# Optimization experiments

Hardware: AMD Instinct MI355X
Metric: run time of the kernel (lower is better)

## Reference

```python
import jax, jax.numpy as jnp
import numpy as np

E = 1024      # embed_dim
H = 16        # num_heads
DH = E // H   # head_dim = 64
B, T = 2, 2048


def setup_inputs() -> dict:
    key = jax.random.key(0)
    ks = jax.random.split(key, 9)
    s = 0.02
    return {
        "hidden_states": jax.random.normal(ks[0], (B, T, E), dtype=jnp.float32),
        "Wq": jax.random.normal(ks[1], (E, E), dtype=jnp.float32) * s,
        "bq": jax.random.normal(ks[2], (E,), dtype=jnp.float32) * s,
        "Wk": jax.random.normal(ks[3], (E, E), dtype=jnp.float32) * s,
        "bk": jax.random.normal(ks[4], (E,), dtype=jnp.float32) * s,
        "Wv": jax.random.normal(ks[5], (E, E), dtype=jnp.float32) * s,
        "bv": jax.random.normal(ks[6], (E,), dtype=jnp.float32) * s,
        "Wo": jax.random.normal(ks[7], (E, E), dtype=jnp.float32) * s,
        "bo": jax.random.normal(ks[8], (E,), dtype=jnp.float32) * s,
    }


def reference(hidden_states, Wq, bq, Wk, bk, Wv, bv, Wo, bo):
    # Faithful to the source, including its bugs:
    #  - q scaled by head_dim**-0.5 AND scores divided by sqrt(head_dim) -> net 1/head_dim
    #  - softmax output assigned to a dead variable; raw scores used for AV matmul
    b, t, _ = hidden_states.shape
    scaling = DH ** -0.5
    q = (hidden_states @ Wq.T + bq) * scaling            # [b, t, E]
    k = hidden_states @ Wk.T + bk
    v = hidden_states @ Wv.T + bv

    def split_heads(x):  # [b, t, E] -> [b, H, t, DH]
        return x.reshape(b, t, H, DH).transpose(0, 2, 1, 3)

    qh, kh, vh = split_heads(q), split_heads(k), split_heads(v)
    attn = jnp.einsum("bhtd,bhsd->bhts", qh, kh) / jnp.sqrt(jnp.float32(DH))
    # (softmax computed in source but its result is discarded)
    out = jnp.einsum("bhts,bhsd->bhtd", attn, vh)        # [b, H, t, DH]
    out = out.transpose(0, 2, 1, 3).reshape(b, t, E)
    return out @ Wo.T + bo
```

## Files before the change

kernel.cpp:

```cpp
#include <hip/hip_runtime.h>

#define E_  1024
#define H_  16
#define B_  2
#define T_  2048
#define BT_ (B_*T_)

typedef __bf16 bf16x8 __attribute__((ext_vector_type(8)));
typedef float  f32x4  __attribute__((ext_vector_type(4)));
typedef unsigned short u16x8 __attribute__((ext_vector_type(8)));

static __device__ __forceinline__ unsigned short f2bf(float x){
  unsigned int u = __float_as_uint(x);
  u += 0x7fffu + ((u >> 16) & 1u);
  return (unsigned short)(u >> 16);
}
static __device__ __forceinline__ float bf2f(unsigned short s){
  return __uint_as_float(((unsigned int)s) << 16);
}

static __device__ __forceinline__ void gld16(const unsigned short* g, unsigned short* l){
  __builtin_amdgcn_global_load_lds(
      (const __attribute__((address_space(1))) void*)g,
      (__attribute__((address_space(3))) void*)l, 16, 0, 0);
}

__global__ __launch_bounds__(256)
void cast_all(const float* __restrict__ hidden,
              const float* __restrict__ Wq, const float* __restrict__ Wk,
              const float* __restrict__ Wv, const float* __restrict__ Wo,
              unsigned short* __restrict__ hb,
              unsigned short* __restrict__ wqkv, unsigned short* __restrict__ wob){
  int bid = blockIdx.x;
  const float* src;
  unsigned short* dst;
  int off;
  if (bid < 2048) {
    src = hidden; dst = hb; off = bid * 2048 + threadIdx.x * 8;
  } else {
    int w = (bid - 2048) >> 9;
    off = ((bid - 2048) & 511) * 2048 + threadIdx.x * 8;
    src = (w==0) ? Wq : (w==1) ? Wk : (w==2) ? Wv : Wo;
    dst = (w==3) ? wob : (wqkv + (size_t)w * 1048576);
  }
  float4 v0 = *(const float4*)(src + off);
  float4 v1 = *(const float4*)(src + off + 4);
  u16x8 o;
  o[0]=f2bf(v0.x); o[1]=f2bf(v0.y); o[2]=f2bf(v0.z); o[3]=f2bf(v0.w);
  o[4]=f2bf(v1.x); o[5]=f2bf(v1.y); o[6]=f2bf(v1.z); o[7]=f2bf(v1.w);
  *(u16x8*)(dst + off) = o;
}

__global__ __launch_bounds__(256)
void gemm_qkv(const unsigned short* __restrict__ A,
              const unsigned short* __restrict__ Wqkv,
              const float* __restrict__ bq, const float* __restrict__ bk,
              const float* __restrict__ bv,
              unsigned short* __restrict__ Q, unsigned short* __restrict__ Ko,
              unsigned short* __restrict__ Vo)
{
  __shared__ unsigned short As[4096];
  __shared__ unsigned short Bs[4096];
  const int tid = threadIdx.x;
  const int wv = tid >> 6, ln = tid & 63;
  const int wr = wv >> 1, wc = wv & 1;
  const int lr = ln & 15;
  const int lk8 = (ln >> 4) * 8;
  const int bm = blockIdx.x, bn = blockIdx.y;
  const size_t arow0 = (size_t)bm * 128;
  const size_t brow0 = (size_t)bn * 128;
  const int K = 1024;

  f32x4 acc[4][4];
  #pragma unroll
  for (int m = 0; m < 4; ++m)
    #pragma unroll
    for (int n = 0; n < 4; ++n) acc[m][n] = (f32x4){0.f,0.f,0.f,0.f};

  for (int k0 = 0; k0 < K; k0 += 32) {
    #pragma unroll
    for (int i = 0; i < 2; ++i) {
      int c = i*256 + wv*64 + ln;
      int row = c >> 2, off = (c & 3) * 8;
      gld16(A    + (arow0 + row) * K + k0 + off, As + (size_t)(i*256 + wv*64) * 8);
      gld16(Wqkv + (brow0 + row) * K + k0 + off, Bs + (size_t)(i*256 + wv*64) * 8);
    }
    __syncthreads();
    bf16x8 af[4], bf[4];
    #pragma unroll
    for (int m = 0; m < 4; ++m) af[m] = *(const bf16x8*)&As[(wr*64 + m*16 + lr)*32 + lk8];
    #pragma unroll
    for (int n = 0; n < 4; ++n) bf[n] = *(const bf16x8*)&Bs[(wc*64 + n*16 + lr)*32 + lk8];
    #pragma unroll
    for (int m = 0; m < 4; ++m)
      #pragma unroll
      for (int n = 0; n < 4; ++n)
        acc[m][n] = __builtin_amdgcn_mfma_f32_16x16x32_bf16(af[m], bf[n], acc[m][n], 0, 0, 0);
    __syncthreads();
  }

  const int which = bn >> 3;
  const float* bias = (which==0) ? bq : (which==1) ? bk : bv;
  unsigned short* Out = (which==0) ? Q : (which==1) ? Ko : Vo;
  const float scale = (which==0) ? 0.125f : 1.0f;
  #pragma unroll
  for (int n = 0; n < 4; ++n) {
    int col = (bn & 7)*128 + wc*64 + n*16 + lr;
    float bvv = bias[col];
    #pragma unroll
    for (int m = 0; m < 4; ++m) {
      int row0 = bm*128 + wr*64 + m*16 + (ln >> 4) * 4;
      #pragma unroll
      for (int r = 0; r < 4; ++r)
        Out[(size_t)(row0 + r) * 1024 + col] = f2bf((acc[m][n][r] + bvv) * scale);
    }
  }
}

__global__ __launch_bounds__(256)
void gemm_o(const unsigned short* __restrict__ A,
            const unsigned short* __restrict__ Bw,
            const float* __restrict__ bias, float* __restrict__ C)
{
  __shared__ unsigned short As[4096];
  __shared__ unsigned short Bs[2048];
  const int tid = threadIdx.x;
  const int wv = tid >> 6, ln = tid & 63;
  const int wr = wv >> 1, wc = wv & 1;
  const int lr = ln & 15;
  const int lk8 = (ln >> 4) * 8;
  const int bm = blockIdx.x, bn = blockIdx.y;
  const size_t arow0 = (size_t)bm * 128;
  const size_t brow0 = (size_t)bn * 64;
  const int K = 1024;

  f32x4 acc[4][2];
  #pragma unroll
  for (int m = 0; m < 4; ++m)
    #pragma unroll
    for (int n = 0; n < 2; ++n) acc[m][n] = (f32x4){0.f,0.f,0.f,0.f};

  for (int k0 = 0; k0 < K; k0 += 32) {
    #pragma unroll
    for (int i = 0; i < 2; ++i) {
      int c = i*256 + wv*64 + ln;
      int row = c >> 2, off = (c & 3) * 8;
      gld16(A + (arow0 + row) * K + k0 + off, As + (size_t)(i*256 + wv*64) * 8);
    }
    { int c = wv*64 + ln; int row = c >> 2, off = (c & 3) * 8;
      gld16(Bw + (brow0 + row) * K + k0 + off, Bs + (size_t)(wv*64) * 8); }
    __syncthreads();
    bf16x8 af[4], bf[2];
    #pragma unroll
    for (int m = 0; m < 4; ++m) af[m] = *(const bf16x8*)&As[(wr*64 + m*16 + lr)*32 + lk8];
    #pragma unroll
    for (int n = 0; n < 2; ++n) bf[n] = *(const bf16x8*)&Bs[(wc*32 + n*16 + lr)*32 + lk8];
    #pragma unroll
    for (int m = 0; m < 4; ++m)
      #pragma unroll
      for (int n = 0; n < 2; ++n)
        acc[m][n] = __builtin_amdgcn_mfma_f32_16x16x32_bf16(af[m], bf[n], acc[m][n], 0, 0, 0);
    __syncthreads();
  }

  #pragma unroll
  for (int n = 0; n < 2; ++n) {
    int col = bn*64 + wc*32 + n*16 + lr;
    float bvv = bias[col];
    #pragma unroll
    for (int m = 0; m < 4; ++m) {
      int row0 = bm*128 + wr*64 + m*16 + (ln >> 4) * 4;
      #pragma unroll
      for (int r = 0; r < 4; ++r)
        C[(size_t)(row0 + r) * 1024 + col] = acc[m][n][r] + bvv;
    }
  }
}

__global__ __launch_bounds__(256)
void ktv_partial(const unsigned short* __restrict__ Kmat,
                 const unsigned short* __restrict__ Vmat,
                 float* __restrict__ Mpart)
{
  __shared__ float Ks[32][64];
  __shared__ float Vs[32][64];
  const int tid   = threadIdx.x;
  const int bh    = blockIdx.x;
  const int chunk = blockIdx.y;
  const int b = bh >> 4, h = bh & 15;
  const int d2  = tid & 63;
  const int d1b = (tid >> 6) * 16;
  float acc[16];
  #pragma unroll
  for (int i = 0; i < 16; ++i) acc[i] = 0.f;
  const int row = tid >> 3, off = (tid & 7) * 8;
  const size_t base = ((size_t)b * T_) * E_ + (size_t)h * 64;

  for (int t0 = chunk * 128; t0 < chunk * 128 + 128; t0 += 32) {
    u16x8 kv = *(const u16x8*)(Kmat + base + (size_t)(t0 + row) * E_ + off);
    u16x8 vv = *(const u16x8*)(Vmat + base + (size_t)(t0 + row) * E_ + off);
    #pragma unroll
    for (int j = 0; j < 8; ++j) { Ks[row][off+j] = bf2f(kv[j]); Vs[row][off+j] = bf2f(vv[j]); }
    __syncthreads();
    for (int tt = 0; tt < 32; ++tt) {
      float vvv = Vs[tt][d2];
      #pragma unroll
      for (int i = 0; i < 16; ++i) acc[i] += Ks[tt][d1b + i] * vvv;
    }
    __syncthreads();
  }
  float* mp = Mpart + ((size_t)bh * 16 + chunk) * 4096;
  #pragma unroll
  for (int i = 0; i < 16; ++i) mp[(d1b + i) * 64 + d2] = acc[i];
}

__global__ __launch_bounds__(256)
void ktv_reduce(const float* __restrict__ Mpart, float* __restrict__ Mfin){
  const int bh = blockIdx.x;
  for (int i = threadIdx.x; i < 4096; i += 256) {
    float s = 0.f;
    #pragma unroll
    for (int c = 0; c < 16; ++c) s += Mpart[((size_t)bh * 16 + c) * 4096 + i];
    Mfin[(size_t)bh * 4096 + i] = s * 0.125f;
  }
}

__global__ __launch_bounds__(256)
void qm_kernel(const unsigned short* __restrict__ Q,
               const float* __restrict__ Mfin,
               unsigned short* __restrict__ O)
{
  __shared__ float Ms[64][64];
  __shared__ float Qs[32][64];
  const int tid = threadIdx.x;
  const int rb  = blockIdx.x;
  const int h   = blockIdx.y;
  const int b   = rb >> 6;
  const int t0  = (rb & 63) * 32;
  const float* mf = Mfin + ((size_t)(b * 16 + h)) * 4096;
  for (int i = tid; i < 4096; i += 256) Ms[i >> 6][i & 63] = mf[i];
  const int row = tid >> 3, off = (tid & 7) * 8;
  const size_t base = ((size_t)b * T_) * E_ + (size_t)h * 64;
  u16x8 qv = *(const u16x8*)(Q + base + (size_t)(t0 + row) * E_ + off);
  #pragma unroll
  for (int j = 0; j < 8; ++j) Qs[row][off + j] = bf2f(qv[j]);
  __syncthreads();
  const int d2 = tid & 63;
  const int r0 = (tid >> 6) * 8;
  for (int rr = r0; rr < r0 + 8; ++rr) {
    float s = 0.f;
    #pragma unroll
    for (int d1 = 0; d1 < 64; ++d1) s += Qs[rr][d1] * Ms[d1][d2];
    O[base + (size_t)(t0 + rr) * E_ + d2] = f2bf(s);
  }
}

extern "C" void kernel_launch(void* const* d_in, const int* in_sizes, int n_in,
                              void* d_out, int out_size, void* d_ws, size_t ws_size,
                              hipStream_t stream)
{
  const float* hidden = (const float*)d_in[0];
  const float* Wq = (const float*)d_in[1];
  const float* bq = (const float*)d_in[2];
  const float* Wk = (const float*)d_in[3];
  const float* bk = (const float*)d_in[4];
  const float* Wv = (const float*)d_in[5];
  const float* bv = (const float*)d_in[6];
  const float* Wo = (const float*)d_in[7];
  const float* bo = (const float*)d_in[8];
  float* out = (float*)d_out;

  const size_t SZ_ACT = (size_t)BT_ * E_;
  const size_t SZ_W   = (size_t)E_ * E_;

  char* p = (char*)d_ws;
  unsigned short* hb   = (unsigned short*)p; p += SZ_ACT * 2;
  unsigned short* wqkv = (unsigned short*)p; p += SZ_W * 3 * 2;
  unsigned short* wob  = (unsigned short*)p; p += SZ_W * 2;
  unsigned short* qb   = (unsigned short*)p; p += SZ_ACT * 2;
  unsigned short* kb   = (unsigned short*)p; p += SZ_ACT * 2;
  unsigned short* vb   = (unsigned short*)p; p += SZ_ACT * 2;
  unsigned short* ob   = (unsigned short*)p; p += SZ_ACT * 2;
  float* Mpart = (float*)p; p += (size_t)32 * 16 * 4096 * 4;
  float* Mfin  = (float*)p; p += (size_t)32 * 4096 * 4;

  cast_all<<<4096, 256, 0, stream>>>(hidden, Wq, Wk, Wv, Wo, hb, wqkv, wob);

  gemm_qkv<<<dim3(32, 24), 256, 0, stream>>>(hb, wqkv, bq, bk, bv, qb, kb, vb);

  ktv_partial<<<dim3(32, 16), 256, 0, stream>>>(kb, vb, Mpart);
  ktv_reduce <<<32, 256, 0, stream>>>(Mpart, Mfin);
  qm_kernel  <<<dim3(128, 16), 256, 0, stream>>>(qb, Mfin, ob);

  gemm_o<<<dim3(32, 16), 256, 0, stream>>>(ob, wob, bo, out);
}
```

Before: 106.0 us.

## Use bf16 MFMA for Q·M product with transposed bf16 M matrix

The reduce kernel now writes the final per-head 64x64 K^T V matrix transposed and rounded to bf16, staged through a padded LDS tile. The Q·M kernel drops its LDS staging and scalar FMA loop. Each wave instead loads Q and M^T fragments directly from global memory and issues 16x16x32 bf16 MFMA instructions. This removes LDS traffic and scalar compute in that stage, at the cost of an extra bf16 rounding of M that may add numerical error.

```diff
diff --git a/kernel.cpp b/kernel.cpp
--- a/kernel.cpp
+++ b/kernel.cpp
@@ -215,43 +215,66 @@
 }
 
 __global__ __launch_bounds__(256)
-void ktv_reduce(const float* __restrict__ Mpart, float* __restrict__ Mfin){
+void ktv_reduce(const float* __restrict__ Mpart, unsigned short* __restrict__ MfinT){
+  __shared__ float Tl[64][65];
   const int bh = blockIdx.x;
-  for (int i = threadIdx.x; i < 4096; i += 256) {
+  const int tid = threadIdx.x;
+  #pragma unroll
+  for (int j = 0; j < 16; ++j) {
+    int i = j*256 + tid;
     float s = 0.f;
     #pragma unroll
     for (int c = 0; c < 16; ++c) s += Mpart[((size_t)bh * 16 + c) * 4096 + i];
-    Mfin[(size_t)bh * 4096 + i] = s * 0.125f;
+    Tl[i & 63][i >> 6] = s * 0.125f;
+  }
+  __syncthreads();
+  unsigned short* o = MfinT + (size_t)bh * 4096;
+  #pragma unroll
+  for (int j = 0; j < 16; ++j) {
+    int i = j*256 + tid;
+    o[i] = f2bf(Tl[i >> 6][i & 63]);
   }
 }
 
 __global__ __launch_bounds__(256)
 void qm_kernel(const unsigned short* __restrict__ Q,
-               const float* __restrict__ Mfin,
+               const unsigned short* __restrict__ MfinT,
                unsigned short* __restrict__ O)
 {
-  __shared__ float Ms[64][64];
-  __shared__ float Qs[32][64];
   const int tid = threadIdx.x;
-  const int rb  = blockIdx.x;
-  const int h   = blockIdx.y;
-  const int b   = rb >> 6;
-  const int t0  = (rb & 63) * 32;
-  const float* mf = Mfin + ((size_t)(b * 16 + h)) * 4096;
-  for (int i = tid; i < 4096; i += 256) Ms[i >> 6][i & 63] = mf[i];
-  const int row = tid >> 3, off = (tid & 7) * 8;
+  const int wv = tid >> 6, ln = tid & 63;
+  const int lr = ln & 15, lk8 = (ln >> 4) * 8;
+  const int rb = blockIdx.x;
+  const int h  = blockIdx.y;
+  const int b  = rb >> 6;
+  const int t0 = (rb & 63) * 32;
   const size_t base = ((size_t)b * T_) * E_ + (size_t)h * 64;
-  u16x8 qv = *(const u16x8*)(Q + base + (size_t)(t0 + row) * E_ + off);
-  #pragma unroll
-  for (int j = 0; j < 8; ++j) Qs[row][off + j] = bf2f(qv[j]);
-  __syncthreads();
-  const int d2 = tid & 63;
-  const int r0 = (tid >> 6) * 8;
-  for (int rr = r0; rr < r0 + 8; ++rr) {
-    float s = 0.f;
-    #pragma unroll
-    for (int d1 = 0; d1 < 64; ++d1) s += Qs[rr][d1] * Ms[d1][d2];
-    O[base + (size_t)(t0 + rr) * E_ + d2] = f2bf(s);
+  const unsigned short* mt = MfinT + ((size_t)(b * 16 + h)) * 4096;
+
+  bf16x8 af[2][2], bf[2];
+  #pragma unroll
+  for (int m = 0; m < 2; ++m)
+    #pragma unroll
+    for (int kk = 0; kk < 2; ++kk)
+      af[m][kk] = *(const bf16x8*)(Q + base + (size_t)(t0 + m*16 + lr) * E_ + kk*32 + lk8);
+  #pragma unroll
+  for (int kk = 0; kk < 2; ++kk)
+    bf[kk] = *(const bf16x8*)(mt + (wv*16 + lr) * 64 + kk*32 + lk8);
+
+  f32x4 acc[2] = {(f32x4){0.f,0.f,0.f,0.f}, (f32x4){0.f,0.f,0.f,0.f}};
+  #pragma unroll
+  for (int m = 0; m < 2; ++m)
+    #pragma unroll
+    for (int kk = 0; kk < 2; ++kk)
+      acc[m] = __builtin_amdgcn_mfma_f32_16x16x32_bf16(af[m][kk], bf[kk], acc[m], 0, 0, 0);
+
+  const int col = wv*16 + lr;
+  #pragma unroll
+  for (int m = 0; m < 2; ++m) {
+    int row0 = t0 + m*16 + (ln >> 4) * 4;
+    #pragma unroll
+    for (int r = 0; r < 4; ++r)
+      O[base + (size_t)(row0 + r) * E_ + col] = f2bf(acc[m][r]);
   }
 }
 
@@ -274,23 +297,23 @@
   const size_t SZ_W   = (size_t)E_ * E_;
 
   char* p = (char*)d_ws;
-  unsigned short* hb   = (unsigned short*)p; p += SZ_ACT * 2;
-  unsigned short* wqkv = (unsigned short*)p; p += SZ_W * 3 * 2;
-  unsigned short* wob  = (unsigned short*)p; p += SZ_W * 2;
-  unsigned short* qb   = (unsigned short*)p; p += SZ_ACT * 2;
-  unsigned short* kb   = (unsigned short*)p; p += SZ_ACT * 2;
-  unsigned short* vb   = (unsigned short*)p; p += SZ_ACT * 2;
-  unsigned short* ob   = (unsigned short*)p; p += SZ_ACT * 2;
+  unsigned short* hb    = (unsigned short*)p; p += SZ_ACT * 2;
+  unsigned short* wqkv  = (unsigned short*)p; p += SZ_W * 3 * 2;
+  unsigned short* wob   = (unsigned short*)p; p += SZ_W * 2;
+  unsigned short* qb    = (unsigned short*)p; p += SZ_ACT * 2;
+  unsigned short* kb    = (unsigned short*)p; p += SZ_ACT * 2;
+  unsigned short* vb    = (unsigned short*)p; p += SZ_ACT * 2;
+  unsigned short* ob    = (unsigned short*)p; p += SZ_ACT * 2;
   float* Mpart = (float*)p; p += (size_t)32 * 16 * 4096 * 4;
-  float* Mfin  = (float*)p; p += (size_t)32 * 4096 * 4;
+  unsigned short* MfinT = (unsigned short*)p; p += (size_t)32 * 4096 * 2;
 
   cast_all<<<4096, 256, 0, stream>>>(hidden, Wq, Wk, Wv, Wo, hb, wqkv, wob);
 
   gemm_qkv<<<dim3(32, 24), 256, 0, stream>>>(hb, wqkv, bq, bk, bv, qb, kb, vb);
 
   ktv_partial<<<dim3(32, 16), 256, 0, stream>>>(kb, vb, Mpart);
-  ktv_reduce <<<32, 256, 0, stream>>>(Mpart, Mfin);
-  qm_kernel  <<<dim3(128, 16), 256, 0, stream>>>(qb, Mfin, ob);
+  ktv_reduce <<<32, 256, 0, stream>>>(Mpart, MfinT);
+  qm_kernel  <<<dim3(128, 16), 256, 0, stream>>>(qb, MfinT, ob);
 
   gemm_o<<<dim3(32, 16), 256, 0, stream>>>(ob, wob, bo, out);
 }
```

Measured after the change: 92.53 us, median of 3. 12.7% less time.
